# Kernel tuning notes

Measured on AMD Instinct MI355X. Metric: run time of the kernel, lower is better.

Reference implementation:

```python
import jax, jax.numpy as jnp
import numpy as np

B, N, D, H, E = 32, 512, 512, 8, 4
HD = D // H
EPS = 1e-3  # keras LayerNormalization default epsilon
NEG = -1e9  # keras Softmax masking additive constant


def _ln(x, g, b):
    m = jnp.mean(x, axis=-1, keepdims=True)
    v = jnp.mean(jnp.square(x - m), axis=-1, keepdims=True)
    return (x - m) * jax.lax.rsqrt(v + EPS) * g + b


def setup_inputs() -> dict:
    key = jax.random.key(0)
    ks = jax.random.split(key, 16)
    s = 0.02
    return {
        "x": jax.random.normal(ks[0], (B, N, D), jnp.float32),
        "mask": jax.random.randint(ks[1], (B, 1, N, N), 0, 2) > 0,
        "interaction": jax.random.normal(ks[2], (B, N, N, H), jnp.float32),
        "w_qkv": jax.random.normal(ks[3], (D, 3 * D), jnp.float32) * s,
        "b_qkv": jnp.zeros((3 * D,), jnp.float32),
        "w_out": jax.random.normal(ks[4], (D, D), jnp.float32) * s,
        "b_out": jnp.zeros((D,), jnp.float32),
        "w1": jax.random.normal(ks[5], (D, E * D), jnp.float32) * s,
        "b1": jnp.zeros((E * D,), jnp.float32),
        "w2": jax.random.normal(ks[6], (E * D, D), jnp.float32) * s,
        "b2": jnp.zeros((D,), jnp.float32),
        "g_pre": jnp.ones((D,), jnp.float32), "be_pre": jnp.zeros((D,), jnp.float32),
        "g_post": jnp.ones((D,), jnp.float32), "be_post": jnp.zeros((D,), jnp.float32),
        "g_ffn": jnp.ones((D,), jnp.float32), "be_ffn": jnp.zeros((D,), jnp.float32),
        "g_mid": jnp.ones((E * D,), jnp.float32), "be_mid": jnp.zeros((E * D,), jnp.float32),
    }


def reference(x, mask, interaction, w_qkv, b_qkv, w_out, b_out, w1, b1, w2, b2,
              g_pre, be_pre, g_post, be_post, g_ffn, be_ffn, g_mid, be_mid):
    # pre-LN MHSA
    h = _ln(x, g_pre, be_pre)
    qkv = h @ w_qkv + b_qkv                           # [B,N,3D]
    qkv = qkv.reshape(B, N, 3, H, HD)
    q, k, v = (jnp.transpose(qkv[:, :, i], (0, 2, 1, 3)) for i in range(3))  # [B,H,N,HD]
    scores = jnp.einsum('bhnd,bhmd->bhnm', q, k) / np.sqrt(HD).astype(np.float32)
    scores = scores + jnp.transpose(interaction, (0, 3, 1, 2))  # per-head additive bias
    scores = scores + (1.0 - mask.astype(scores.dtype)) * NEG   # keras Softmax mask semantics
    attn = jax.nn.softmax(scores, axis=-1)
    o = jnp.einsum('bhnm,bhmd->bhnd', attn, v)
    o = jnp.transpose(o, (0, 2, 1, 3)).reshape(B, N, D)
    o = o @ w_out + b_out
    attended = _ln(o, g_post, be_post) + x            # post-MHSA LN then residual
    # FFN with mid-LN
    f = _ln(attended, g_ffn, be_ffn)
    f = jax.nn.gelu(f @ w1 + b1, approximate=False)
    f = _ln(f, g_mid, be_mid)
    f = f @ w2 + b2
    return f + attended
```

## Files before the change

kernel.cpp:

```cpp
#include <hip/hip_runtime.h>
#include <hip/hip_bf16.h>
#include <math.h>

constexpr int CB = 32, CN = 512, CD = 512, CH = 8, CHD = 64;
constexpr float LN_EPS = 1e-3f;

typedef _Float16 half8 __attribute__((ext_vector_type(8)));
typedef float f32x4 __attribute__((ext_vector_type(4)));

__device__ __forceinline__ void async16(const void* g, void* l) {
    __builtin_amdgcn_global_load_lds((const __attribute__((address_space(1))) void*)g,
                                     (__attribute__((address_space(3))) void*)l, 16, 0, 0);
}

__global__ __launch_bounds__(256) void transpose_f16(const float* __restrict__ in,
                                                     _Float16* __restrict__ out,
                                                     int K, int N) {
    __shared__ float t[32][33];
    const int tx = threadIdx.x % 32, ty = threadIdx.x / 32;
    const int n0 = blockIdx.x * 32, k0 = blockIdx.y * 32;
#pragma unroll
    for (int i = 0; i < 4; ++i)
        t[ty + i * 8][tx] = in[(size_t)(k0 + ty + i * 8) * N + n0 + tx];
    __syncthreads();
#pragma unroll
    for (int i = 0; i < 4; ++i)
        out[(size_t)(n0 + ty + i * 8) * K + k0 + tx] = (_Float16)t[tx][ty + i * 8];
}

template<int WIDTH, bool IN_F16, bool OUT_F16, bool ADDRES>
__global__ __launch_bounds__(256) void ln2_kernel(const void* __restrict__ in_,
        const float* __restrict__ g, const float* __restrict__ be,
        const float* __restrict__ res, void* __restrict__ out_) {
    constexpr int NPL = WIDTH / 64;
    const int row = blockIdx.x * 4 + (threadIdx.x >> 6);
    const int lane = threadIdx.x & 63;
    const int c0 = lane * NPL;
    float v[NPL];
    if (IN_F16) {
        const _Float16* p = (const _Float16*)in_ + (size_t)row * WIDTH + c0;
#pragma unroll
        for (int i = 0; i < NPL / 8; ++i) {
            half8 u = *(const half8*)(p + i * 8);
#pragma unroll
            for (int j = 0; j < 8; ++j) v[i * 8 + j] = (float)u[j];
        }
    } else {
        const float* p = (const float*)in_ + (size_t)row * WIDTH + c0;
#pragma unroll
        for (int i = 0; i < NPL / 4; ++i) {
            float4 u = *(const float4*)(p + i * 4);
            v[i * 4 + 0] = u.x; v[i * 4 + 1] = u.y; v[i * 4 + 2] = u.z; v[i * 4 + 3] = u.w;
        }
    }
    float s1 = 0.f, s2 = 0.f;
#pragma unroll
    for (int i = 0; i < NPL; ++i) { s1 += v[i]; s2 += v[i] * v[i]; }
#pragma unroll
    for (int off = 1; off < 64; off <<= 1) { s1 += __shfl_xor(s1, off); s2 += __shfl_xor(s2, off); }
    const float mean = s1 * (1.0f / WIDTH);
    const float var = s2 * (1.0f / WIDTH) - mean * mean;
    const float rstd = rsqrtf(var + LN_EPS);

    float ov[NPL];
#pragma unroll
    for (int i = 0; i < NPL / 4; ++i) {
        float4 gv = *(const float4*)(g + c0 + i * 4);
        float4 bv = *(const float4*)(be + c0 + i * 4);
        ov[i * 4 + 0] = (v[i * 4 + 0] - mean) * rstd * gv.x + bv.x;
        ov[i * 4 + 1] = (v[i * 4 + 1] - mean) * rstd * gv.y + bv.y;
        ov[i * 4 + 2] = (v[i * 4 + 2] - mean) * rstd * gv.z + bv.z;
        ov[i * 4 + 3] = (v[i * 4 + 3] - mean) * rstd * gv.w + bv.w;
    }
    if (ADDRES) {
        const float* rp = res + (size_t)row * WIDTH + c0;
#pragma unroll
        for (int i = 0; i < NPL / 4; ++i) {
            float4 rv = *(const float4*)(rp + i * 4);
            ov[i * 4 + 0] += rv.x; ov[i * 4 + 1] += rv.y; ov[i * 4 + 2] += rv.z; ov[i * 4 + 3] += rv.w;
        }
    }
    if (OUT_F16) {
        _Float16* po = (_Float16*)out_ + (size_t)row * WIDTH + c0;
#pragma unroll
        for (int i = 0; i < NPL / 8; ++i) {
            half8 hv;
#pragma unroll
            for (int j = 0; j < 8; ++j) hv[j] = (_Float16)ov[i * 8 + j];
            *(half8*)(po + i * 8) = hv;
        }
    } else {
        float* po = (float*)out_ + (size_t)row * WIDTH + c0;
#pragma unroll
        for (int i = 0; i < NPL / 4; ++i) {
            float4 w = make_float4(ov[i * 4 + 0], ov[i * 4 + 1], ov[i * 4 + 2], ov[i * 4 + 3]);
            *(float4*)(po + i * 4) = w;
        }
    }
}

__global__ __launch_bounds__(256) void ln_post_ffn(const _Float16* __restrict__ o2,
        const float* __restrict__ x,
        const float* __restrict__ g_post, const float* __restrict__ be_post,
        const float* __restrict__ g_ffn, const float* __restrict__ be_ffn,
        float* __restrict__ attended, _Float16* __restrict__ f) {
    constexpr int NPL = 8;
    const int row = blockIdx.x * 4 + (threadIdx.x >> 6);
    const int lane = threadIdx.x & 63;
    const int c0 = lane * NPL;
    float v[NPL], xv[NPL];
    {
        half8 u = *(const half8*)(o2 + (size_t)row * CD + c0);
#pragma unroll
        for (int j = 0; j < 8; ++j) v[j] = (float)u[j];
        float4 a = *(const float4*)(x + (size_t)row * CD + c0);
        float4 b = *(const float4*)(x + (size_t)row * CD + c0 + 4);
        xv[0] = a.x; xv[1] = a.y; xv[2] = a.z; xv[3] = a.w;
        xv[4] = b.x; xv[5] = b.y; xv[6] = b.z; xv[7] = b.w;
    }
    float s1 = 0.f, s2 = 0.f;
#pragma unroll
    for (int i = 0; i < NPL; ++i) { s1 += v[i]; s2 += v[i] * v[i]; }
#pragma unroll
    for (int off = 1; off < 64; off <<= 1) { s1 += __shfl_xor(s1, off); s2 += __shfl_xor(s2, off); }
    float mean = s1 * (1.0f / CD);
    float rstd = rsqrtf(s2 * (1.0f / CD) - mean * mean + LN_EPS);
    float av[NPL];
#pragma unroll
    for (int i = 0; i < NPL; ++i)
        av[i] = (v[i] - mean) * rstd * g_post[c0 + i] + be_post[c0 + i] + xv[i];
    {
        float4 w0 = make_float4(av[0], av[1], av[2], av[3]);
        float4 w1 = make_float4(av[4], av[5], av[6], av[7]);
        *(float4*)(attended + (size_t)row * CD + c0) = w0;
        *(float4*)(attended + (size_t)row * CD + c0 + 4) = w1;
    }
    s1 = 0.f; s2 = 0.f;
#pragma unroll
    for (int i = 0; i < NPL; ++i) { s1 += av[i]; s2 += av[i] * av[i]; }
#pragma unroll
    for (int off = 1; off < 64; off <<= 1) { s1 += __shfl_xor(s1, off); s2 += __shfl_xor(s2, off); }
    mean = s1 * (1.0f / CD);
    rstd = rsqrtf(s2 * (1.0f / CD) - mean * mean + LN_EPS);
    half8 hv;
#pragma unroll
    for (int i = 0; i < NPL; ++i)
        hv[i] = (_Float16)((av[i] - mean) * rstd * g_ffn[c0 + i] + be_ffn[c0 + i]);
    *(half8*)(f + (size_t)row * CD + c0) = hv;
}

template<bool GELU, bool RES, bool OUT_F16>
__global__ __launch_bounds__(256) void gemm_f16(const _Float16* __restrict__ A,
        const _Float16* __restrict__ Wt, const float* __restrict__ bias,
        const float* __restrict__ res, void* __restrict__ Cout,
        int M, int N, int K) {
    __shared__ __align__(16) char As[16384];
    __shared__ __align__(16) char Bs[16384];
    const int tid = threadIdx.x;
    const int nbx = N >> 7;
    const int nwg = (M >> 7) * nbx;
    int gb = blockIdx.x;
    gb = (gb & 7) * (nwg >> 3) + (gb >> 3);
    const int by = gb / nbx, bx = gb % nbx;

    const int lane = tid & 63;
    const int wv = tid >> 6;
    const int rsub = lane >> 3;
    const int slot = lane & 7;
    const int chunk = slot ^ rsub;
    const _Float16* Abase = A + (size_t)(by * 128) * K + chunk * 8;
    const _Float16* Bbase = Wt + (size_t)(bx * 128) * K + chunk * 8;

    const int wm = wv >> 1, wn = wv & 1;
    const int lrow = lane & 15;
    const int lk = lane >> 4;
    const int xorv = lane & 7;
    const int aRowB = (wm * 64 + lrow) * 128;
    const int bRowB = (wn * 64 + lrow) * 128;

    f32x4 acc[4][4] = {};

    for (int k0 = 0; k0 < K; k0 += 64) {
#pragma unroll
        for (int t = 0; t < 4; ++t) {
            const int rowb = t * 32 + wv * 8;
            async16(Abase + (size_t)(rowb + rsub) * K + k0, As + rowb * 128);
            async16(Bbase + (size_t)(rowb + rsub) * K + k0, Bs + rowb * 128);
        }
        __syncthreads();
#pragma unroll
        for (int kk = 0; kk < 2; ++kk) {
            const int sa = ((kk * 4 + lk) ^ xorv) << 4;
            half8 af[4], bf[4];
#pragma unroll
            for (int mi = 0; mi < 4; ++mi) af[mi] = *(const half8*)(As + aRowB + mi * 2048 + sa);
#pragma unroll
            for (int ni = 0; ni < 4; ++ni) bf[ni] = *(const half8*)(Bs + bRowB + ni * 2048 + sa);
#pragma unroll
            for (int mi = 0; mi < 4; ++mi)
#pragma unroll
                for (int ni = 0; ni < 4; ++ni)
                    acc[mi][ni] = __builtin_amdgcn_mfma_f32_16x16x32_f16(af[mi], bf[ni], acc[mi][ni], 0, 0, 0);
        }
        __syncthreads();
    }

    const int lr4 = (lane >> 4) * 4;
    const int lc = lane & 15;
#pragma unroll
    for (int ni = 0; ni < 4; ++ni) {
        const int colg = bx * 128 + wn * 64 + ni * 16 + lc;
        const float bv = bias[colg];
#pragma unroll
        for (int mi = 0; mi < 4; ++mi) {
            const int rowg = by * 128 + wm * 64 + mi * 16 + lr4;
#pragma unroll
            for (int r = 0; r < 4; ++r) {
                float v = acc[mi][ni][r] + bv;
                if (GELU) v = 0.5f * v * (1.0f + erff(v * 0.70710678118654752440f));
                if (RES) v += res[(size_t)(rowg + r) * N + colg];
                if (OUT_F16) ((_Float16*)Cout)[(size_t)(rowg + r) * N + colg] = (_Float16)v;
                else ((float*)Cout)[(size_t)(rowg + r) * N + colg] = v;
            }
        }
    }
}

__global__ __launch_bounds__(256) void attn_mfma(
        const _Float16* __restrict__ qkv, const float* __restrict__ inter,
        const int* __restrict__ mask, _Float16* __restrict__ o) {
    const int bid = blockIdx.x;
    const int xcd = bid & 7;
    const int s = bid >> 3;
    const int h = s & 7;
    const int qt = (s >> 3) & 7;
    const int b = (s >> 6) * 8 + xcd;
    const int tid = threadIdx.x;
    const int lane = tid & 63;
    const int w = tid >> 6;
    const int l15 = lane & 15, l4 = lane >> 4;

    __shared__ __align__(16) char Qs[8192];
    __shared__ __align__(16) char Ks[8192];
    __shared__ __align__(16) char Vt[8192];
    __shared__ __align__(16) char Ps[8192];

    constexpr size_t QKVROW = 1536;
    {
        const _Float16* Qg = qkv + (size_t)(b * CN + qt * 64) * QKVROW + h * 64;
#pragma unroll
        for (int p = 0; p < 2; ++p) {
            const int f = tid + 256 * p;
            const int r = f >> 3, c = f & 7;
            half8 v = *(const half8*)(Qg + (size_t)r * QKVROW + c * 8);
            *(half8*)(Qs + r * 128 + ((c ^ (r & 7)) << 4)) = v;
        }
    }

    f32x4 acc_o[4] = {};
    float m_run[4] = {-3e38f, -3e38f, -3e38f, -3e38f};
    float l_run[4] = {0.f, 0.f, 0.f, 0.f};

    const int qg0 = qt * 64 + w * 16 + l4 * 4;
    const float* interB[4];
    const int* maskB[4];
#pragma unroll
    for (int r = 0; r < 4; ++r) {
        interB[r] = inter + ((size_t)(b * CN + qg0 + r) * CN) * CH + h;
        maskB[r]  = mask + (size_t)(b * CN + qg0 + r) * CN;
    }

    for (int mt = 0; mt < 8; ++mt) {
        __syncthreads();
        const _Float16* Kg = qkv + (size_t)(b * CN + mt * 64) * QKVROW + 512 + h * 64;
        const _Float16* Vg = Kg + 512;
#pragma unroll
        for (int p = 0; p < 2; ++p) {
            const int f = tid + 256 * p;
            const int r = f >> 3, c = f & 7;
            half8 kv = *(const half8*)(Kg + (size_t)r * QKVROW + c * 8);
            *(half8*)(Ks + r * 128 + ((c ^ (r & 7)) << 4)) = kv;
        }
#pragma unroll
        for (int p = 0; p < 2; ++p) {
            const int f = tid + 256 * p;
            const int m = f >> 3, dc = f & 7;
            half8 vv = *(const half8*)(Vg + (size_t)m * QKVROW + dc * 8);
            const int mc = m >> 3, mo = m & 7;
#pragma unroll
            for (int j = 0; j < 8; ++j) {
                const int d = dc * 8 + j;
                *(_Float16*)(Vt + d * 128 + ((mc ^ (d & 7) ^ dc) << 4) + mo * 2) = vv[j];
            }
        }
        float iv[4][4];
#pragma unroll
        for (int r = 0; r < 4; ++r)
#pragma unroll
            for (int mi = 0; mi < 4; ++mi) {
                const int m = mt * 64 + mi * 16 + l15;
                const float bvv = interB[r][(size_t)m * CH];
                iv[r][mi] = bvv + (maskB[r][m] ? 0.f : -1e9f);
            }
        __syncthreads();

        f32x4 acc_s[4] = {};
#pragma unroll
        for (int step = 0; step < 2; ++step) {
            const int qrow = w * 16 + l15;
            const int ch = step * 4 + l4;
            half8 aq = *(const half8*)(Qs + qrow * 128 + ((ch ^ (qrow & 7)) << 4));
#pragma unroll
            for (int mi = 0; mi < 4; ++mi) {
                const int mrow = mi * 16 + l15;
                half8 bk = *(const half8*)(Ks + mrow * 128 + ((ch ^ (mrow & 7)) << 4));
                acc_s[mi] = __builtin_amdgcn_mfma_f32_16x16x32_f16(aq, bk, acc_s[mi], 0, 0, 0);
            }
        }
#pragma unroll
        for (int r = 0; r < 4; ++r) {
            float pv[4];
            float rmax = -3e38f;
#pragma unroll
            for (int mi = 0; mi < 4; ++mi) {
                float sv = acc_s[mi][r] * 0.125f + iv[r][mi];
                pv[mi] = sv;
                rmax = fmaxf(rmax, sv);
            }
#pragma unroll
            for (int off = 1; off < 16; off <<= 1) rmax = fmaxf(rmax, __shfl_xor(rmax, off));
            const float nm = fmaxf(m_run[r], rmax);
            const float fac = __expf(m_run[r] - nm);
            m_run[r] = nm;
            float ps = 0.f;
#pragma unroll
            for (int mi = 0; mi < 4; ++mi) { float e = __expf(pv[mi] - nm); pv[mi] = e; ps += e; }
#pragma unroll
            for (int off = 1; off < 16; off <<= 1) ps += __shfl_xor(ps, off);
            l_run[r] = l_run[r] * fac + ps;
#pragma unroll
            for (int di = 0; di < 4; ++di) acc_o[di][r] *= fac;
            const int qrow = w * 16 + l4 * 4 + r;
#pragma unroll
            for (int mi = 0; mi < 4; ++mi) {
                const int m = mi * 16 + l15;
                *(_Float16*)(Ps + qrow * 128 + (((m >> 3) ^ (qrow & 7)) << 4) + (m & 7) * 2) = (_Float16)pv[mi];
            }
        }
#pragma unroll
        for (int step = 0; step < 2; ++step) {
            const int qrow = w * 16 + l15;
            const int ch = step * 4 + l4;
            half8 ap = *(const half8*)(Ps + qrow * 128 + ((ch ^ (qrow & 7)) << 4));
#pragma unroll
            for (int di = 0; di < 4; ++di) {
                const int drow = di * 16 + l15;
                half8 bv = *(const half8*)(Vt + drow * 128 + ((ch ^ (drow & 7) ^ (drow >> 3)) << 4));
                acc_o[di] = __builtin_amdgcn_mfma_f32_16x16x32_f16(ap, bv, acc_o[di], 0, 0, 0);
            }
        }
    }
    _Float16* orow = o + (size_t)(b * CN + qt * 64 + w * 16 + l4 * 4) * CD + h * 64 + l15;
#pragma unroll
    for (int r = 0; r < 4; ++r) {
        const float inv = 1.0f / l_run[r];
#pragma unroll
        for (int di = 0; di < 4; ++di)
            orow[(size_t)r * CD + di * 16] = (_Float16)(acc_o[di][r] * inv);
    }
}

extern "C" void kernel_launch(void* const* d_in, const int* in_sizes, int n_in,
                              void* d_out, int out_size, void* d_ws, size_t ws_size,
                              hipStream_t stream) {
    const float* x      = (const float*)d_in[0];
    const int*   mask   = (const int*)d_in[1];
    const float* inter  = (const float*)d_in[2];
    const float* w_qkv  = (const float*)d_in[3];
    const float* b_qkv  = (const float*)d_in[4];
    const float* w_out  = (const float*)d_in[5];
    const float* b_out  = (const float*)d_in[6];
    const float* w1     = (const float*)d_in[7];
    const float* b1     = (const float*)d_in[8];
    const float* w2     = (const float*)d_in[9];
    const float* b2     = (const float*)d_in[10];
    const float* g_pre  = (const float*)d_in[11];
    const float* be_pre = (const float*)d_in[12];
    const float* g_post = (const float*)d_in[13];
    const float* be_post= (const float*)d_in[14];
    const float* g_ffn  = (const float*)d_in[15];
    const float* be_ffn = (const float*)d_in[16];
    const float* g_mid  = (const float*)d_in[17];
    const float* be_mid = (const float*)d_in[18];
    float* out = (float*)d_out;

    char* ws = (char*)d_ws;
    const size_t MB = 1ull << 20;
    _Float16* wt_qkv = (_Float16*)(ws + 0 * MB);
    _Float16* wt_out = (_Float16*)(ws + 2 * MB);
    _Float16* wt_w1  = (_Float16*)(ws + 3 * MB);
    _Float16* wt_w2  = (_Float16*)(ws + 5 * MB);
    float*    attended = (float*)(ws + 8 * MB);
    _Float16* o2h    = (_Float16*)(ws + 40 * MB);
    _Float16* f1b    = (_Float16*)(ws + 64 * MB);
    _Float16* qkvb   = (_Float16*)(ws + 128 * MB);
    _Float16* hb     = (_Float16*)(ws + 176 * MB);
    _Float16* ob     = (_Float16*)(ws + 192 * MB);
    _Float16* fb     = (_Float16*)(ws + 208 * MB);

    const int M = CB * CN;

    transpose_f16<<<dim3(1536 / 32, 512 / 32), 256, 0, stream>>>(w_qkv, wt_qkv, 512, 1536);
    transpose_f16<<<dim3(512 / 32, 512 / 32), 256, 0, stream>>>(w_out, wt_out, 512, 512);
    transpose_f16<<<dim3(2048 / 32, 512 / 32), 256, 0, stream>>>(w1, wt_w1, 512, 2048);
    transpose_f16<<<dim3(512 / 32, 2048 / 32), 256, 0, stream>>>(w2, wt_w2, 2048, 512);

    ln2_kernel<512, false, true, false><<<M / 4, 256, 0, stream>>>(x, g_pre, be_pre, nullptr, hb);
    gemm_f16<false, false, true><<<(M / 128) * (1536 / 128), 256, 0, stream>>>(
        hb, wt_qkv, b_qkv, nullptr, qkvb, M, 1536, 512);
    attn_mfma<<<CB * 8 * 8, 256, 0, stream>>>(qkvb, inter, mask, ob);
    gemm_f16<false, false, true><<<(M / 128) * (512 / 128), 256, 0, stream>>>(
        ob, wt_out, b_out, nullptr, o2h, M, 512, 512);
    ln_post_ffn<<<M / 4, 256, 0, stream>>>(o2h, x, g_post, be_post, g_ffn, be_ffn, attended, fb);
    gemm_f16<true, false, true><<<(M / 128) * (2048 / 128), 256, 0, stream>>>(
        fb, wt_w1, b1, nullptr, f1b, M, 2048, 512);
    ln2_kernel<2048, true, true, false><<<M / 4, 256, 0, stream>>>(f1b, g_mid, be_mid, nullptr, f1b);
    gemm_f16<false, true, false><<<(M / 128) * (512 / 128), 256, 0, stream>>>(
        f1b, wt_w2, b2, attended, out, M, 512, 2048);
}
```

Baseline: 461.2 us.

## Double-buffer LDS tiles in f16 GEMM to overlap global loads with MFMA

```diff
diff --git a/kernel.cpp b/kernel.cpp
--- a/kernel.cpp
+++ b/kernel.cpp
@@ -154,8 +154,8 @@
         const _Float16* __restrict__ Wt, const float* __restrict__ bias,
         const float* __restrict__ res, void* __restrict__ Cout,
         int M, int N, int K) {
-    __shared__ __align__(16) char As[16384];
-    __shared__ __align__(16) char Bs[16384];
+    __shared__ __align__(16) char As[2][16384];
+    __shared__ __align__(16) char Bs[2][16384];
     const int tid = threadIdx.x;
     const int nbx = N >> 7;
     const int nwg = (M >> 7) * nbx;
@@ -180,29 +180,42 @@
 
     f32x4 acc[4][4] = {};
 
-    for (int k0 = 0; k0 < K; k0 += 64) {
+    auto stage = [&](int buf, int k0) {
 #pragma unroll
         for (int t = 0; t < 4; ++t) {
             const int rowb = t * 32 + wv * 8;
-            async16(Abase + (size_t)(rowb + rsub) * K + k0, As + rowb * 128);
-            async16(Bbase + (size_t)(rowb + rsub) * K + k0, Bs + rowb * 128);
-        }
-        __syncthreads();
+            async16(Abase + (size_t)(rowb + rsub) * K + k0, As[buf] + rowb * 128);
+            async16(Bbase + (size_t)(rowb + rsub) * K + k0, Bs[buf] + rowb * 128);
+        }
+    };
+
+    const int nsteps = K >> 6;
+    stage(0, 0);
+    for (int step = 0; step < nsteps; ++step) {
+        const int cur = step & 1;
+        if (step + 1 < nsteps) {
+            stage(cur ^ 1, (step + 1) * 64);
+            asm volatile("s_waitcnt vmcnt(8)" ::: "memory");
+        } else {
+            asm volatile("s_waitcnt vmcnt(0)" ::: "memory");
+        }
+        __builtin_amdgcn_s_barrier();
 #pragma unroll
         for (int kk = 0; kk < 2; ++kk) {
             const int sa = ((kk * 4 + lk) ^ xorv) << 4;
             half8 af[4], bf[4];
 #pragma unroll
-            for (int mi = 0; mi < 4; ++mi) af[mi] = *(const half8*)(As + aRowB + mi * 2048 + sa);
-#pragma unroll
-            for (int ni = 0; ni < 4; ++ni) bf[ni] = *(const half8*)(Bs + bRowB + ni * 2048 + sa);
+            for (int mi = 0; mi < 4; ++mi) af[mi] = *(const half8*)(As[cur] + aRowB + mi * 2048 + sa);
+#pragma unroll
+            for (int ni = 0; ni < 4; ++ni) bf[ni] = *(const half8*)(Bs[cur] + bRowB + ni * 2048 + sa);
 #pragma unroll
             for (int mi = 0; mi < 4; ++mi)
 #pragma unroll
                 for (int ni = 0; ni < 4; ++ni)
                     acc[mi][ni] = __builtin_amdgcn_mfma_f32_16x16x32_f16(af[mi], bf[ni], acc[mi][ni], 0, 0, 0);
         }
-        __syncthreads();
+        asm volatile("s_waitcnt lgkmcnt(0)" ::: "memory");
+        __builtin_amdgcn_s_barrier();
     }
 
     const int lr4 = (lane >> 4) * 4;
```

Measured after the change: 439.4 us, median of 2. 1.05x faster.
